# Kernel tuning notes

Hardware: AMD Instinct MI355X
Metric: run time of the kernel (lower is better)

## Reference

```python
import jax, jax.numpy as jnp
import numpy as np

SHAPES = (64, 64, 64)
RANGES = np.array([[0.0, 1.0], [0.0, 1.0], [0.0, 1.0]], dtype=np.float32)


def setup_inputs() -> dict:
    key = jax.random.key(0)
    kx, kz = jax.random.split(key)
    B, P = 64, 4096
    x = jax.random.normal(kx, (B,) + SHAPES, dtype=jnp.float32)
    z = jax.random.uniform(kz, (B, P, len(SHAPES)), dtype=jnp.float32)
    return {"x": x, "z": z}


def _points_to_image(z, shapes, ranges):
    # z: [B, P, D] coordinates -> counts: [B, *shapes] histogram
    B, P, D = z.shape
    lo = jnp.asarray(ranges[:, 0])          # [D]
    hi = jnp.asarray(ranges[:, 1])          # [D]
    dims = jnp.asarray(shapes, dtype=jnp.int32)  # [D]
    # bin index per dim, clipped into the grid
    idx = jnp.floor((z - lo) / (hi - lo) * dims.astype(z.dtype)).astype(jnp.int32)
    idx = jnp.clip(idx, 0, dims - 1)        # [B, P, D]
    # linearize 3D bin index
    strides = jnp.asarray(
        [shapes[1] * shapes[2], shapes[2], 1], dtype=jnp.int32
    )
    lin = jnp.sum(idx * strides, axis=-1)   # [B, P]
    G = shapes[0] * shapes[1] * shapes[2]
    counts = jnp.zeros((B, G), dtype=jnp.float32)
    counts = counts.at[jnp.arange(B)[:, None], lin].add(1.0)
    return counts.reshape((B,) + tuple(shapes))


def reference(x, z):
    counts = _points_to_image(z, SHAPES, RANGES)     # [B, 64, 64, 64]
    # cumsum=True branch: reverse inclusive cumulative sum along last dim
    counts = counts + jnp.sum(counts, axis=-1, keepdims=True) - jnp.cumsum(counts, axis=-1)
    mask = (counts > 0).astype(x.dtype)
    r_masked = x * mask
    return counts, r_masked
```

## Files before the change

kernel.cpp:

```cpp
#include <hip/hip_runtime.h>

#define BB 64
#define NDIM 64
#define GRID3 (NDIM * NDIM * NDIM)
#define NPTS 4096

__global__ __launch_bounds__(256) void fused_kernel(const float* __restrict__ x,
                                                    const float* __restrict__ z,
                                                    float* __restrict__ counts,
                                                    float* __restrict__ rm) {
    __shared__ unsigned int H[NDIM * NDIM];

    const int slab = blockIdx.x;
    const int b    = blockIdx.y;
    const int tid  = threadIdx.x;

    uint4* H4 = (uint4*)H;
    #pragma unroll
    for (int i = 0; i < 4; ++i) H4[tid + i * 256] = make_uint4(0u, 0u, 0u, 0u);
    __syncthreads();

    const float* zb = z + (size_t)b * NPTS * 3;
    float z0v[16];
    #pragma unroll
    for (int i = 0; i < 16; ++i) z0v[i] = zb[(size_t)(i * 256 + tid) * 3];

    #pragma unroll
    for (int i = 0; i < 16; ++i) {
        int i0 = min(max((int)floorf(z0v[i] * 64.0f), 0), 63);
        if (i0 == slab) {
            int p = i * 256 + tid;
            float z1 = zb[p * 3 + 1];
            float z2 = zb[p * 3 + 2];
            int i1 = min(max((int)floorf(z1 * 64.0f), 0), 63);
            int i2 = min(max((int)floorf(z2 * 64.0f), 0), 63);
            atomicAdd(&H[(i1 << 6) | i2], 1u);
        }
    }
    __syncthreads();

    {
        const int row = tid >> 2;
        const int seg = tid & 3;
        const int q4  = (row << 4) + (seg << 2);

        float e[16], pr[16];
        #pragma unroll
        for (int i = 0; i < 4; ++i) {
            uint4 q = H4[q4 + i];
            e[4*i+0] = (float)q.x; e[4*i+1] = (float)q.y;
            e[4*i+2] = (float)q.z; e[4*i+3] = (float)q.w;
        }
        float p = 0.0f;
        #pragma unroll
        for (int j = 0; j < 16; ++j) { p += e[j]; pr[j] = p; }
        const float seg_sum = p;

        float sc = seg_sum;
        float n1 = __shfl_up(sc, 1, 4); if ((tid & 3) >= 1) sc += n1;
        float n2 = __shfl_up(sc, 2, 4); if ((tid & 3) >= 2) sc += n2;
        const float T       = __shfl(sc, 3, 4);
        const float segExcl = sc - seg_sum;

        float4* Hf4 = (float4*)H;
        #pragma unroll
        for (int i = 0; i < 4; ++i) {
            float4 w;
            w.x = e[4*i+0] + T - (segExcl + pr[4*i+0]);
            w.y = e[4*i+1] + T - (segExcl + pr[4*i+1]);
            w.z = e[4*i+2] + T - (segExcl + pr[4*i+2]);
            w.w = e[4*i+3] + T - (segExcl + pr[4*i+3]);
            Hf4[q4 + i] = w;
        }
    }
    __syncthreads();

    const int lane = tid & 63;
    const int wave = tid >> 6;
    const float* Hf = (const float*)H;
    const size_t base = ((size_t)b << 18) + ((size_t)slab << 12) + ((size_t)wave << 10);

    #pragma unroll
    for (int r = 0; r < 16; ++r) {
        float s = Hf[((wave * 16 + r) << 6) | lane];
        size_t idx = base + (r << 6) + lane;
        counts[idx] = s;
        float xv = 0.0f;
        if (s > 0.0f) xv = x[idx];
        rm[idx] = xv;
    }
}

extern "C" void kernel_launch(void* const* d_in, const int* in_sizes, int n_in,
                              void* d_out, int out_size, void* d_ws, size_t ws_size,
                              hipStream_t stream) {
    const float* x = (const float*)d_in[0];
    const float* z = (const float*)d_in[1];

    float* counts = (float*)d_out;
    float* rm     = counts + (size_t)BB * GRID3;

    dim3 grid(NDIM, BB);
    fused_kernel<<<grid, 256, 0, stream>>>(x, z, counts, rm);
}
```

Baseline: 209.0 us.

## Pre-bin points per slab in a separate kernel and vectorize output stores

Adds a bin_kernel that computes each point's bin once and appends a packed 16-bit (i1,i2) index to a per-(batch,slab) list in workspace, with global atomics to claim slots. Each fused-kernel block now reads only the points that fall in its slab instead of scanning all 4096 points of its batch. The write phase is also vectorized to float4 loads and stores. The cost is an extra memset and kernel launch plus global atomics. The float4 path loads x only when s.x>0, which relies on the reverse cumsum being non-increasing along the row.

```diff
diff --git a/kernel.cpp b/kernel.cpp
--- a/kernel.cpp
+++ b/kernel.cpp
@@ -5,8 +5,25 @@
 #define GRID3 (NDIM * NDIM * NDIM)
 #define NPTS 4096
 
+
+__global__ __launch_bounds__(256) void bin_kernel(const float* __restrict__ z,
+                                                  unsigned int* __restrict__ cnt,
+                                                  unsigned short* __restrict__ list) {
+    int t = blockIdx.x * 256 + threadIdx.x;
+    int b = t >> 12;
+    const float* zp = z + (size_t)t * 3;
+    float z0 = zp[0], z1 = zp[1], z2 = zp[2];
+    int i0 = min(max((int)floorf(z0 * 64.0f), 0), 63);
+    int i1 = min(max((int)floorf(z1 * 64.0f), 0), 63);
+    int i2 = min(max((int)floorf(z2 * 64.0f), 0), 63);
+    int sb = (b << 6) | i0;
+    unsigned int slot = atomicAdd(&cnt[sb], 1u);
+    list[((size_t)sb << 12) | slot] = (unsigned short)((i1 << 6) | i2);
+}
+
 __global__ __launch_bounds__(256) void fused_kernel(const float* __restrict__ x,
-                                                    const float* __restrict__ z,
+                                                    const unsigned int* __restrict__ cnt,
+                                                    const unsigned short* __restrict__ list,
                                                     float* __restrict__ counts,
                                                     float* __restrict__ rm) {
     __shared__ unsigned int H[NDIM * NDIM];
@@ -14,29 +31,17 @@
     const int slab = blockIdx.x;
     const int b    = blockIdx.y;
     const int tid  = threadIdx.x;
+    const int sb   = (b << 6) | slab;
 
     uint4* H4 = (uint4*)H;
     #pragma unroll
     for (int i = 0; i < 4; ++i) H4[tid + i * 256] = make_uint4(0u, 0u, 0u, 0u);
     __syncthreads();
 
-    const float* zb = z + (size_t)b * NPTS * 3;
-    float z0v[16];
-    #pragma unroll
-    for (int i = 0; i < 16; ++i) z0v[i] = zb[(size_t)(i * 256 + tid) * 3];
-
-    #pragma unroll
-    for (int i = 0; i < 16; ++i) {
-        int i0 = min(max((int)floorf(z0v[i] * 64.0f), 0), 63);
-        if (i0 == slab) {
-            int p = i * 256 + tid;
-            float z1 = zb[p * 3 + 1];
-            float z2 = zb[p * 3 + 2];
-            int i1 = min(max((int)floorf(z1 * 64.0f), 0), 63);
-            int i2 = min(max((int)floorf(z2 * 64.0f), 0), 63);
-            atomicAdd(&H[(i1 << 6) | i2], 1u);
-        }
-    }
+    const int n = (int)cnt[sb];
+    const unsigned short* lp = list + ((size_t)sb << 12);
+    for (int p = tid; p < n; p += 256)
+        atomicAdd(&H[lp[p]], 1u);
     __syncthreads();
 
     {
@@ -57,8 +62,8 @@
         const float seg_sum = p;
 
         float sc = seg_sum;
-        float n1 = __shfl_up(sc, 1, 4); if ((tid & 3) >= 1) sc += n1;
-        float n2 = __shfl_up(sc, 2, 4); if ((tid & 3) >= 2) sc += n2;
+        float n1 = __shfl_up(sc, 1, 4); if (seg >= 1) sc += n1;
+        float n2 = __shfl_up(sc, 2, 4); if (seg >= 2) sc += n2;
         const float T       = __shfl(sc, 3, 4);
         const float segExcl = sc - seg_sum;
 
@@ -75,19 +80,26 @@
     }
     __syncthreads();
 
-    const int lane = tid & 63;
-    const int wave = tid >> 6;
-    const float* Hf = (const float*)H;
-    const size_t base = ((size_t)b << 18) + ((size_t)slab << 12) + ((size_t)wave << 10);
+    const float4* Hs = (const float4*)H;
+    const float4* x4 = (const float4*)x;
+    float4* c4 = (float4*)counts;
+    float4* r4 = (float4*)rm;
+    const size_t base4 = ((size_t)b << 16) + ((size_t)slab << 10);
 
     #pragma unroll
-    for (int r = 0; r < 16; ++r) {
-        float s = Hf[((wave * 16 + r) << 6) | lane];
-        size_t idx = base + (r << 6) + lane;
-        counts[idx] = s;
-        float xv = 0.0f;
-        if (s > 0.0f) xv = x[idx];
-        rm[idx] = xv;
+    for (int i = 0; i < 4; ++i) {
+        int j = tid + i * 256;
+        float4 s = Hs[j];
+        size_t idx = base4 + j;
+        c4[idx] = s;
+        float4 xv = make_float4(0.f, 0.f, 0.f, 0.f);
+        if (s.x > 0.0f) xv = x4[idx];
+        float4 r;
+        r.x = (s.x > 0.0f) ? xv.x : 0.0f;
+        r.y = (s.y > 0.0f) ? xv.y : 0.0f;
+        r.z = (s.z > 0.0f) ? xv.z : 0.0f;
+        r.w = (s.w > 0.0f) ? xv.w : 0.0f;
+        r4[idx] = r;
     }
 }
 
@@ -100,6 +112,13 @@
     float* counts = (float*)d_out;
     float* rm     = counts + (size_t)BB * GRID3;
 
+    unsigned int*   cnt  = (unsigned int*)d_ws;
+    unsigned short* list = (unsigned short*)((char*)d_ws + 16384);
+
+    hipMemsetAsync(cnt, 0, BB * 64 * sizeof(unsigned int), stream);
+
+    bin_kernel<<<(BB * NPTS) / 256, 256, 0, stream>>>(z, cnt, list);
+
     dim3 grid(NDIM, BB);
-    fused_kernel<<<grid, 256, 0, stream>>>(x, z, counts, rm);
+    fused_kernel<<<grid, 256, 0, stream>>>(x, cnt, list, counts, rm);
 }
```

New measurement: 195.5 us. 6.5% less time.
